# Optimization experiments

Hardware: AMD Instinct MI355X
Metric: run time of the kernel (lower is better)

The kernel has to match this reference:

```python
import jax, jax.numpy as jnp
import numpy as np
import math

EPS = 1e-6


def setup_inputs() -> dict:
    key = jax.random.key(0)
    ks = jax.random.split(key, 6)
    Bsz, S, d_in, d_out, E, r = 4, 2048, 2048, 2048, 16, 16
    x = jax.random.normal(ks[0], (Bsz, S, d_in), dtype=jnp.float32)
    base_W = jax.random.normal(ks[1], (d_out, d_in), dtype=jnp.float32) * (1.0 / math.sqrt(d_in))
    base_b = jax.random.normal(ks[2], (d_out,), dtype=jnp.float32)
    A = jax.random.normal(ks[3], (E, r, d_in), dtype=jnp.float32) * (1.0 / math.sqrt(d_in))
    B = jax.random.normal(ks[4], (E, d_out, r), dtype=jnp.float32) * (1.0 / math.sqrt(r))
    gate_v = jax.random.normal(ks[5], (E, d_in), dtype=jnp.float32)
    alphas = jnp.full((E,), 32.0, dtype=jnp.float32)
    return {"x": x, "base_W": base_W, "base_b": base_b, "A": A, "B": B,
            "gate_v": gate_v, "alphas": alphas, "top_k": 2}


def reference(x, base_W, base_b, A, B, gate_v, alphas, top_k):
    d = x.shape[-1]
    out_shape = x.shape[:-1] + (base_W.shape[0],)
    base_out = jnp.einsum('bsd,od->bso', x, base_W) + base_b

    x_flat = x.reshape(-1, d)                                  # [T, d]
    T = x_flat.shape[0]
    E = A.shape[0]
    # cosine routing scores
    xn = x_flat / (jnp.linalg.norm(x_flat, axis=-1, keepdims=True) + EPS)
    vn = gate_v / (jnp.linalg.norm(gate_v, axis=-1, keepdims=True) + EPS)
    scores = (xn @ vn.T) / jnp.sqrt(jnp.float32(d))            # [T, E]
    topk_s, topk_i = jax.lax.top_k(scores, top_k)              # [T, k]
    w = jax.nn.softmax(topk_s, axis=-1)                        # [T, k]
    # dense combine weight per (token, expert); non-selected experts get 0
    Wte = jnp.zeros((T, E), dtype=x.dtype).at[jnp.arange(T)[:, None], topk_i].add(w)
    scale = alphas / jnp.float32(A.shape[1])                   # [E]
    # grouped LoRA: mid [T,E,r] is tiny (r=16); contract without [T,E,out]
    mid = jnp.einsum('td,erd->ter', x_flat, A)
    contrib = jnp.einsum('ter,eor,te,e->to', mid, B, Wte, scale)
    return base_out + contrib.reshape(out_shape)
```

## Files before the change

### kernel.cpp

```cpp
#include <hip/hip_runtime.h>
#include <math.h>


typedef unsigned short u16;
typedef __attribute__((ext_vector_type(8))) short short8;
typedef __attribute__((ext_vector_type(4))) float floatx4;

#define DEV __device__ __forceinline__

DEV u16 f2b(float f) { unsigned int u; __builtin_memcpy(&u, &f, 4); u += 0x7fffu + ((u >> 16) & 1u); return (u16)(u >> 16); }
DEV float ldf(const float* __restrict__ p, long long i, long long n) { if (i < 0 || i >= n) i = 0; return p[i]; }

DEV void async_cp16(const void* g, void* l) {
  __builtin_amdgcn_global_load_lds(
      (const __attribute__((address_space(1))) unsigned int*)g,
      (__attribute__((address_space(3))) unsigned int*)l, 16, 0, 0);
}

struct Route { int e0, e1; float c0, c1; };

#define MAX_T 8192
#define MAX_K 2048
#define MAX_DOUT 2048
#define MAX_ER 256

__device__ Route g_route[MAX_T];
__device__ float g_vnorm[16];
__device__ float g_mid[(size_t)MAX_T * MAX_ER];
__device__ __align__(16) u16 g_xb[(size_t)MAX_T * MAX_K];
__device__ __align__(16) u16 g_wb[(size_t)MAX_DOUT * MAX_K];
__device__ __align__(16) u16 g_ab[(size_t)MAX_ER * MAX_K];
__device__ __align__(16) u16 g_mw[(size_t)MAX_T * MAX_ER];
__device__ __align__(16) u16 g_w2[(size_t)MAX_DOUT * MAX_ER];

__global__ __launch_bounds__(256) void cvt_bf16(const float* __restrict__ src, long long n, int which) {
  u16* dst; long long cap;
  if (which == 1) { dst = g_wb; cap = (long long)MAX_DOUT * MAX_K; }
  else { dst = g_ab; cap = (long long)MAX_ER * MAX_K; }
  const long long stride = (long long)gridDim.x * 256 * 4;
  for (long long i4 = ((long long)blockIdx.x * 256 + threadIdx.x) * 4; i4 < n; i4 += stride) {
    if (i4 + 4 <= n && i4 + 4 <= cap) {
      const float4 v = *(const float4*)(src + i4);
      ushort4 o;
      o.x = f2b(v.x); o.y = f2b(v.y); o.z = f2b(v.z); o.w = f2b(v.w);
      *(ushort4*)(dst + i4) = o;
    } else {
      for (long long j = i4; j < n && j < cap; ++j) dst[j] = f2b(src[j]);
    }
  }
}

__global__ __launch_bounds__(256) void build_w2(const float* __restrict__ Bw, long long nB,
                                                int d_out, int r, int E, int Er) {
  const int gid = blockIdx.x * 256 + threadIdx.x;
  if (gid >= d_out * E) return;
  const int o = gid / E, e = gid % E;
  const long long src = ((long long)e * d_out + o) * r;
  const long long dst = (long long)o * Er + (long long)e * r;
  if (r == 16 && src + 16 <= nB) {
    short8 lo, hi;
#pragma unroll
    for (int j = 0; j < 8; ++j) lo[j] = (short)f2b(Bw[src + j]);
#pragma unroll
    for (int j = 0; j < 8; ++j) hi[j] = (short)f2b(Bw[src + 8 + j]);
    *(short8*)&g_w2[dst] = lo;
    *(short8*)&g_w2[dst + 8] = hi;
  } else {
    for (int j = 0; j < r; ++j) g_w2[dst + j] = f2b(ldf(Bw, src + j, nB));
  }
}

__global__ __launch_bounds__(64) void gate_norm(const float* __restrict__ gv, long long nG,
                                                int d, int E) {
  const int e = blockIdx.x;
  if (e >= E || e >= 16) return;
  const int lane = threadIdx.x;
  float vv = 0.f;
  const float* gp = gv + (long long)e * d;
  for (int k = lane * 4; k + 4 <= d; k += 256) {
    const float4 g = *(const float4*)(gp + k);
    vv += g.x * g.x + g.y * g.y + g.z * g.z + g.w * g.w;
  }
#pragma unroll
  for (int m = 1; m < 64; m <<= 1) vv += __shfl_xor(vv, m);
  if (lane == 0) g_vnorm[e] = sqrtf(vv) + 1e-6f;
}

__global__ __launch_bounds__(256) void router_cvtx(
    const float* __restrict__ x, long long nX,
    const float* __restrict__ gate_v, long long nG,
    const float* __restrict__ alphas, long long nAl,
    const int* __restrict__ topk_ptr, int has_topk,
    int T, int d, int r, int E) {
  const int wave = threadIdx.x >> 6, lane = threadIdx.x & 63;
  const int t = blockIdx.x * 4 + wave;
  if (t >= T || t >= MAX_T) return;
  float xx = 0.f, dot[16], vv[16];
#pragma unroll
  for (int e = 0; e < 16; ++e) { dot[e] = 0.f; vv[e] = 0.f; }
  const long long xbase = (long long)t * d;
  const int dvec = ((d & 3) == 0) ? d : 0;
  for (int i = lane * 4; i < dvec; i += 256) {
    const float4 xv = *(const float4*)(x + xbase + i);
    xx += xv.x * xv.x + xv.y * xv.y + xv.z * xv.z + xv.w * xv.w;
    ushort4 ob; ob.x = f2b(xv.x); ob.y = f2b(xv.y); ob.z = f2b(xv.z); ob.w = f2b(xv.w);
    *(ushort4*)&g_xb[xbase + i] = ob;
#pragma unroll
    for (int e = 0; e < 16; ++e) {
      if (e < E) {
        const float4 g = *(const float4*)(gate_v + (long long)e * d + i);
        dot[e] += xv.x * g.x + xv.y * g.y + xv.z * g.z + xv.w * g.w;
        vv[e] += g.x * g.x + g.y * g.y + g.z * g.z + g.w * g.w;
      }
    }
  }
  for (int i = dvec + lane; i < d; i += 64) {
    const float xv = ldf(x, xbase + i, nX);
    g_xb[xbase + i] = f2b(xv);
    xx += xv * xv;
#pragma unroll
    for (int e = 0; e < 16; ++e) {
      if (e < E) {
        const float g = ldf(gate_v, (long long)e * d + i, nG);
        dot[e] += xv * g;
        vv[e] += g * g;
      }
    }
  }
#pragma unroll
  for (int m = 1; m < 64; m <<= 1) {
    xx += __shfl_xor(xx, m);
#pragma unroll
    for (int e = 0; e < 16; ++e) {
      dot[e] += __shfl_xor(dot[e], m);
      vv[e] += __shfl_xor(vv[e], m);
    }
  }
  const float inv_sd = 1.0f / sqrtf((float)d);
  const float xnorm = sqrtf(xx) + 1e-6f;
  float s[16];
#pragma unroll
  for (int e = 0; e < 16; ++e)
    s[e] = (e < E) ? dot[e] / (xnorm * (sqrtf(vv[e]) + 1e-6f)) * inv_sd : -1e30f;
  int e0 = 0; float s0 = s[0];
#pragma unroll
  for (int e = 1; e < 16; ++e) if (s[e] > s0) { s0 = s[e]; e0 = e; }
  int e1 = (e0 == 0) ? 1 : 0; float s1 = s[e1];
#pragma unroll
  for (int e = 0; e < 16; ++e) if (e != e0 && s[e] > s1) { s1 = s[e]; e1 = e; }
  const int k = has_topk ? *topk_ptr : 2;
  float w0 = 1.f, w1 = 0.f;
  if (k >= 2) {
    const float ex = expf(s1 - s0);
    w0 = 1.f / (1.f + ex);
    w1 = ex / (1.f + ex);
  } else {
    e1 = e0;
  }
  if (lane == 0) {
    Route rt;
    rt.e0 = e0; rt.e1 = e1;
    rt.c0 = w0 * ldf(alphas, e0, nAl) / (float)r;
    rt.c1 = w1 * ldf(alphas, e1, nAl) / (float)r;
    g_route[t] = rt;
  }
}

__global__ __launch_bounds__(256) void router_lds(
    const float* __restrict__ x, long long nX,
    const float* __restrict__ gate_v, long long nG,
    const float* __restrict__ alphas, long long nAl,
    const int* __restrict__ topk_ptr, int has_topk,
    int T, int d, int r, int E) {
  __shared__ __align__(16) float gls[4096];
  const int tid = threadIdx.x;
  const int w = tid >> 6, lane = tid & 63;
  const int t = blockIdx.x * 4 + w;
  const bool valid = (t < T && t < MAX_T);
  const long long xbase = (long long)t * d;

  float dot[16], xx = 0.f;
#pragma unroll
  for (int e = 0; e < 16; ++e) dot[e] = 0.f;

  for (int k0 = 0; k0 < d; k0 += 256) {
    __syncthreads();
#pragma unroll
    for (int i = 0; i < 4; ++i) {
      const int f = tid * 4 + i * 1024;
      const int e = f >> 8, kk = f & 255;
      float4 g = (float4){0.f, 0.f, 0.f, 0.f};
      if (e < E) g = *(const float4*)(gate_v + (long long)e * d + k0 + kk);
      *(float4*)&gls[f] = g;
    }
    __syncthreads();
    float4 xv = (float4){0.f, 0.f, 0.f, 0.f};
    if (valid) {
      xv = *(const float4*)(x + xbase + k0 + lane * 4);
      ushort4 ob; ob.x = f2b(xv.x); ob.y = f2b(xv.y); ob.z = f2b(xv.z); ob.w = f2b(xv.w);
      *(ushort4*)&g_xb[xbase + k0 + lane * 4] = ob;
    }
    xx += xv.x * xv.x + xv.y * xv.y + xv.z * xv.z + xv.w * xv.w;
#pragma unroll
    for (int e = 0; e < 16; ++e) {
      if (e < E) {
        const float4 g = *(const float4*)&gls[e * 256 + lane * 4];
        dot[e] += xv.x * g.x + xv.y * g.y + xv.z * g.z + xv.w * g.w;
      }
    }
  }
#pragma unroll
  for (int m = 1; m < 64; m <<= 1) {
    xx += __shfl_xor(xx, m);
#pragma unroll
    for (int e = 0; e < 16; ++e) dot[e] += __shfl_xor(dot[e], m);
  }
  if (valid && lane == 0) {
    const float inv_sd = 1.0f / sqrtf((float)d);
    const float xnorm = sqrtf(xx) + 1e-6f;
    float s[16];
#pragma unroll
    for (int e = 0; e < 16; ++e)
      s[e] = (e < E) ? dot[e] / (xnorm * g_vnorm[e]) * inv_sd : -1e30f;
    int e0 = 0; float s0 = s[0];
#pragma unroll
    for (int e = 1; e < 16; ++e) if (s[e] > s0) { s0 = s[e]; e0 = e; }
    int e1 = (e0 == 0) ? 1 : 0; float s1 = s[e1];
#pragma unroll
    for (int e = 0; e < 16; ++e) if (e != e0 && s[e] > s1) { s1 = s[e]; e1 = e; }
    const int k = has_topk ? *topk_ptr : 2;
    float w0 = 1.f, w1 = 0.f;
    if (k >= 2) {
      const float ex = expf(s1 - s0);
      w0 = 1.f / (1.f + ex);
      w1 = ex / (1.f + ex);
    } else {
      e1 = e0;
    }
    Route rt;
    rt.e0 = e0; rt.e1 = e1;
    rt.c0 = w0 * ldf(alphas, e0, nAl) / (float)r;
    rt.c1 = w1 * ldf(alphas, e1, nAl) / (float)r;
    g_route[t] = rt;
  }
}

#define BM 128
#define BN 128
#define BK 32

__global__ __launch_bounds__(256) void gemm_main(
    const float* __restrict__ bias, long long nBias,
    float* __restrict__ Out, long long nOut,
    int K, int d_out, int Er, int T) {
  __shared__ __align__(16) u16 As[BM * BK];
  __shared__ __align__(16) u16 Bs[BN * BK];
  const int tid = threadIdx.x;
  const int w = tid >> 6, lane = tid & 63;
  const int Mb = blockIdx.y * BM;
  const int Nb = blockIdx.x * BN;
  const int wm = w >> 1, wn = w & 1;
  const int chunk0 = w * 2;
  const int srow = lane >> 2;
  const int kb = (lane & 3) * 8;

  floatx4 acc[4][4];
#pragma unroll
  for (int mt = 0; mt < 4; ++mt)
#pragma unroll
    for (int nt = 0; nt < 4; ++nt) acc[mt][nt] = (floatx4){0.f, 0.f, 0.f, 0.f};

  for (int k0 = 0; k0 < K; k0 += BK) {
#pragma unroll
    for (int c = 0; c < 2; ++c) {
      const int row = (chunk0 + c) * 16 + srow;
      async_cp16(g_xb + (size_t)(Mb + row) * K + (k0 + kb), (char*)As + (chunk0 + c) * 1024);
    }
#pragma unroll
    for (int c = 0; c < 2; ++c) {
      const int row = (chunk0 + c) * 16 + srow;
      const int col = Nb + row;
      const u16* g = (col >= d_out) ? g_ab + (size_t)(col - d_out) * K + (k0 + kb)
                                    : g_wb + (size_t)col * K + (k0 + kb);
      async_cp16(g, (char*)Bs + (chunk0 + c) * 1024);
    }
    __syncthreads();
    short8 a[4], b[4];
#pragma unroll
    for (int mt = 0; mt < 4; ++mt)
      a[mt] = *(const short8*)&As[(wm * 64 + mt * 16 + (lane & 15)) * BK + (lane >> 4) * 8];
#pragma unroll
    for (int nt = 0; nt < 4; ++nt)
      b[nt] = *(const short8*)&Bs[(wn * 64 + nt * 16 + (lane & 15)) * BK + (lane >> 4) * 8];
#pragma unroll
    for (int mt = 0; mt < 4; ++mt)
#pragma unroll
      for (int nt = 0; nt < 4; ++nt)
        acc[mt][nt] = __builtin_amdgcn_mfma_f32_16x16x32_bf16(a[mt], b[nt], acc[mt][nt], 0, 0, 0);
    __syncthreads();
  }

  const int colb = Nb + wn * 64 + (lane & 15);
  const int rowb = Mb + wm * 64 + (lane >> 4) * 4;
#pragma unroll
  for (int nt = 0; nt < 4; ++nt) {
    const int col = colb + nt * 16;
    const bool isOut = (col < d_out);
    const float bv = isOut ? ldf(bias, col, nBias) : 0.f;
#pragma unroll
    for (int mt = 0; mt < 4; ++mt) {
      const int row = rowb + mt * 16;
#pragma unroll
      for (int i = 0; i < 4; ++i) {
        const int rr = row + i;
        if (rr >= T) continue;
        if (isOut) {
          const long long idx = (long long)rr * d_out + col;
          if (idx < nOut) Out[idx] = acc[mt][nt][i] + bv;
        } else {
          const int mc = col - d_out;
          if (mc < Er) g_mid[(long long)rr * Er + mc] = acc[mt][nt][i];
        }
      }
    }
  }
}

__global__ __launch_bounds__(256) void build_mw(int T, int r, int Er, int E) {
  const int t = blockIdx.x;
  if (t >= T) return;
  const Route rt = g_route[t];
  for (int j = threadIdx.x; j < Er; j += 256) {
    const int e = (r == 16) ? (j >> 4) : (j / r);
    float wgt = 0.f;
    if (e == rt.e0) wgt = rt.c0;
    else if (e == rt.e1) wgt = rt.c1;
    g_mw[(long long)t * Er + j] = f2b(wgt * g_mid[(long long)t * Er + j]);
  }
}

__global__ __launch_bounds__(256) void gemm_lora(
    float* __restrict__ Out, long long nOut, int Kc, int d_out, int T) {
  __shared__ __align__(16) u16 As[BM * BK];
  __shared__ __align__(16) u16 Bs[BN * BK];
  const int tid = threadIdx.x;
  const int w = tid >> 6, lane = tid & 63;
  const int Mb = blockIdx.y * BM;
  const int Nb = blockIdx.x * BN;
  const int wm = w >> 1, wn = w & 1;
  const int chunk0 = w * 2;
  const int srow = lane >> 2;
  const int kb = (lane & 3) * 8;

  floatx4 acc[4][4];
#pragma unroll
  for (int mt = 0; mt < 4; ++mt)
#pragma unroll
    for (int nt = 0; nt < 4; ++nt) acc[mt][nt] = (floatx4){0.f, 0.f, 0.f, 0.f};

  for (int k0 = 0; k0 < Kc; k0 += BK) {
#pragma unroll
    for (int c = 0; c < 2; ++c) {
      const int row = (chunk0 + c) * 16 + srow;
      async_cp16(g_mw + (size_t)(Mb + row) * Kc + (k0 + kb), (char*)As + (chunk0 + c) * 1024);
      async_cp16(g_w2 + (size_t)(Nb + row) * Kc + (k0 + kb), (char*)Bs + (chunk0 + c) * 1024);
    }
    __syncthreads();
    short8 a[4], b[4];
#pragma unroll
    for (int mt = 0; mt < 4; ++mt)
      a[mt] = *(const short8*)&As[(wm * 64 + mt * 16 + (lane & 15)) * BK + (lane >> 4) * 8];
#pragma unroll
    for (int nt = 0; nt < 4; ++nt)
      b[nt] = *(const short8*)&Bs[(wn * 64 + nt * 16 + (lane & 15)) * BK + (lane >> 4) * 8];
#pragma unroll
    for (int mt = 0; mt < 4; ++mt)
#pragma unroll
      for (int nt = 0; nt < 4; ++nt)
        acc[mt][nt] = __builtin_amdgcn_mfma_f32_16x16x32_bf16(a[mt], b[nt], acc[mt][nt], 0, 0, 0);
    __syncthreads();
  }

  const int colb = Nb + wn * 64 + (lane & 15);
  const int rowb = Mb + wm * 64 + (lane >> 4) * 4;
#pragma unroll
  for (int nt = 0; nt < 4; ++nt) {
    const int col = colb + nt * 16;
#pragma unroll
    for (int mt = 0; mt < 4; ++mt) {
      const int row = rowb + mt * 16;
#pragma unroll
      for (int i = 0; i < 4; ++i) {
        const int rr = row + i;
        if (rr >= T) continue;
        const long long idx = (long long)rr * d_out + col;
        if (idx < nOut) Out[idx] += acc[mt][nt][i];
      }
    }
  }
}


__global__ __launch_bounds__(256) void gemm_mid(int K, int Er, int T, int r) {
  __shared__ __align__(16) u16 As[BM * BK];
  __shared__ __align__(16) u16 Bs[BN * BK];
  const int tid = threadIdx.x;
  const int w = tid >> 6, lane = tid & 63;
  int lin = blockIdx.y * gridDim.x + blockIdx.x;
  const int nwg = gridDim.x * gridDim.y;
  if ((nwg & 7) == 0) { const int cpx = nwg >> 3; lin = (lin & 7) * cpx + (lin >> 3); }
  const int Mb = (lin / gridDim.x) * BM;
  const int Nb = (lin % gridDim.x) * BN;
  const int wm = w >> 1, wn = w & 1;
  const int chunk0 = w * 2;
  const int srow = lane >> 2;
  const int kb = (lane & 3) * 8;

  floatx4 acc[4][4];
#pragma unroll
  for (int mt = 0; mt < 4; ++mt)
#pragma unroll
    for (int nt = 0; nt < 4; ++nt) acc[mt][nt] = (floatx4){0.f, 0.f, 0.f, 0.f};

  for (int k0 = 0; k0 < K; k0 += BK) {
#pragma unroll
    for (int c = 0; c < 2; ++c) {
      const int row = (chunk0 + c) * 16 + srow;
      async_cp16(g_xb + (size_t)(Mb + row) * K + (k0 + kb), (char*)As + (chunk0 + c) * 1024);
      async_cp16(g_ab + (size_t)(Nb + row) * K + (k0 + kb), (char*)Bs + (chunk0 + c) * 1024);
    }
    __syncthreads();
    short8 a[4], b[4];
#pragma unroll
    for (int mt = 0; mt < 4; ++mt)
      a[mt] = *(const short8*)&As[(wm * 64 + mt * 16 + (lane & 15)) * BK + (lane >> 4) * 8];
#pragma unroll
    for (int nt = 0; nt < 4; ++nt)
      b[nt] = *(const short8*)&Bs[(wn * 64 + nt * 16 + (lane & 15)) * BK + (lane >> 4) * 8];
#pragma unroll
    for (int mt = 0; mt < 4; ++mt)
#pragma unroll
      for (int nt = 0; nt < 4; ++nt)
        acc[mt][nt] = __builtin_amdgcn_mfma_f32_16x16x32_bf16(a[mt], b[nt], acc[mt][nt], 0, 0, 0);
    __syncthreads();
  }

  const int colb = Nb + wn * 64 + (lane & 15);
  const int rowb = Mb + wm * 64 + (lane >> 4) * 4;
#pragma unroll
  for (int mt = 0; mt < 4; ++mt) {
#pragma unroll
    for (int i = 0; i < 4; ++i) {
      const int rr = rowb + mt * 16 + i;
      if (rr >= T) continue;
      const Route rt = g_route[rr];
#pragma unroll
      for (int nt = 0; nt < 4; ++nt) {
        const int col = colb + nt * 16;
        if (col >= Er) continue;
        const int e = (r == 16) ? (col >> 4) : (col / r);
        float wgt = 0.f;
        if (e == rt.e0) wgt = rt.c0;
        else if (e == rt.e1) wgt = rt.c1;
        g_mw[(long long)rr * Er + col] = f2b(wgt * acc[mt][nt][i]);
      }
    }
  }
}

DEV void stage_ht(int tsched, int half, int isB, int NT, int Mb, int Nb,
                  int Kxb, int Er, char* smem, int w, int lane) {
  int t = (tsched < NT) ? tsched : (NT - 1);
  const int k0 = t << 6;
  const u16* src; int stride, col0;
  if (k0 < Kxb) { src = isB ? g_wb : g_xb; stride = Kxb; col0 = k0; }
  else          { src = isB ? g_w2 : g_mw; stride = Er;  col0 = k0 - Kxb; }
  const int rbase = (isB ? Nb : Mb) + (half << 7);
  char* dst = smem + (tsched & 1) * 65536 + isB * 32768 + half * 16384 + (w * 2) * 1024;
  const int row = w * 16 + (lane >> 3);
  const int cs = (((lane & 7) ^ (lane >> 3)) << 3);
#pragma unroll
  for (int c = 0; c < 2; ++c) {
    async_cp16(src + (size_t)(rbase + row + c * 8) * stride + col0 + cs, dst + c * 1024);
  }
}

__global__ __launch_bounds__(512, 2) void gemm_main8(
    const float* __restrict__ bias, long long nBias,
    float* __restrict__ Out, long long nOut,
    int Kxb, int d_out, int Er, int T) {
  __shared__ __align__(16) char smem[131072];
  const int tid = threadIdx.x;
  const int w = tid >> 6, lane = tid & 63;
  const int wm = w >> 2, wn = w & 3;
  const int lane15 = lane & 15, laneHi = lane >> 4, lane7 = lane & 7;
  const int NT = (Kxb + Er) >> 6;

  int lin = blockIdx.y * gridDim.x + blockIdx.x;
  const int nwg = gridDim.x * gridDim.y;
  if ((nwg & 7) == 0) { const int cpx = nwg >> 3; lin = (lin & 7) * cpx + (lin >> 3); }
  const int Nb = (lin % gridDim.x) * 256;
  const int Mb = (lin / gridDim.x) * 256;

  floatx4 acc[8][4];
#pragma unroll
  for (int m = 0; m < 8; ++m)
#pragma unroll
    for (int n = 0; n < 4; ++n) acc[m][n] = (floatx4){0.f, 0.f, 0.f, 0.f};

  stage_ht(0, 0, 0, NT, Mb, Nb, Kxb, Er, smem, w, lane);
  stage_ht(0, 1, 0, NT, Mb, Nb, Kxb, Er, smem, w, lane);
  stage_ht(0, 0, 1, NT, Mb, Nb, Kxb, Er, smem, w, lane);
  stage_ht(0, 1, 1, NT, Mb, Nb, Kxb, Er, smem, w, lane);
  stage_ht(1, 0, 1, NT, Mb, Nb, Kxb, Er, smem, w, lane);
  stage_ht(1, 1, 1, NT, Mb, Nb, Kxb, Er, smem, w, lane);
  asm volatile("s_waitcnt vmcnt(4)" ::: "memory");
  __builtin_amdgcn_s_barrier();
  asm volatile("" ::: "memory");

  const int xorw = lane7 << 4;
  short8 a[2][2], b[4][2];

  for (int t = 0; t < NT; ++t) {
    const int sbase = (t & 1) * 65536;
    const char* Ab = smem + sbase;
    const char* Bb = smem + sbase + 32768;
#pragma unroll
    for (int q = 0; q < 4; ++q) {
      if (q == 0) {
#pragma unroll
        for (int n = 0; n < 4; ++n)
#pragma unroll
          for (int kk = 0; kk < 2; ++kk)
            b[n][kk] = *(const short8*)(Bb + (wn * 64 + n * 16 + lane15) * 128 +
                                        ((kk * 64 + laneHi * 16) ^ xorw));
      }
#pragma unroll
      for (int mm = 0; mm < 2; ++mm)
#pragma unroll
        for (int kk = 0; kk < 2; ++kk)
          a[mm][kk] = *(const short8*)(Ab + (wm * 128 + (2 * q + mm) * 16 + lane15) * 128 +
                                       ((kk * 64 + laneHi * 16) ^ xorw));
      if (q < 2) stage_ht(t + 1, q, 0, NT, Mb, Nb, Kxb, Er, smem, w, lane);
      else       stage_ht(t + 2, q - 2, 1, NT, Mb, Nb, Kxb, Er, smem, w, lane);
      if (q == 3) asm volatile("s_waitcnt vmcnt(4)" ::: "memory");
      __builtin_amdgcn_s_barrier();
      asm volatile("" ::: "memory");
      asm volatile("s_waitcnt lgkmcnt(0)" ::: "memory");
      __builtin_amdgcn_s_setprio(1);
#pragma unroll
      for (int kk = 0; kk < 2; ++kk)
#pragma unroll
        for (int mm = 0; mm < 2; ++mm)
#pragma unroll
          for (int n = 0; n < 4; ++n)
            acc[2 * q + mm][n] =
                __builtin_amdgcn_mfma_f32_16x16x32_bf16(a[mm][kk], b[n][kk], acc[2 * q + mm][n], 0, 0, 0);
      __builtin_amdgcn_s_setprio(0);
      __builtin_amdgcn_s_barrier();
      asm volatile("" ::: "memory");
    }
  }
  asm volatile("s_waitcnt vmcnt(0)" ::: "memory");

  const int colb = Nb + wn * 64 + lane15;
  const int rowb = Mb + wm * 128 + laneHi * 4;
#pragma unroll
  for (int n = 0; n < 4; ++n) {
    const int col = colb + n * 16;
    const float bv = ldf(bias, col, nBias);
#pragma unroll
    for (int m = 0; m < 8; ++m) {
#pragma unroll
      for (int i = 0; i < 4; ++i) {
        const int row = rowb + m * 16 + i;
        const long long idx = (long long)row * d_out + col;
        if (row < T && idx < nOut) Out[idx] = acc[m][n][i] + bv;
      }
    }
  }
}

extern "C" void kernel_launch(void* const* d_in, const int* in_sizes, int n_in,
                              void* d_out, int out_size, void* d_ws, size_t ws_size,
                              hipStream_t stream) {
  if (n_in < 7 || !d_out) return;
  const float* x    = (const float*)d_in[0];
  const float* W    = (const float*)d_in[1];
  const float* bias = (const float*)d_in[2];
  const float* A    = (const float*)d_in[3];
  const float* B    = (const float*)d_in[4];
  const float* gv   = (const float*)d_in[5];
  const float* al   = (const float*)d_in[6];
  const int has_topk = (n_in > 7 && in_sizes[7] >= 1) ? 1 : 0;
  const int* topk = has_topk ? (const int*)d_in[7] : nullptr;
  float* out = (float*)d_out;

  const long long nX = in_sizes[0], nW = in_sizes[1], nBias = in_sizes[2];
  const long long nA = in_sizes[3], nB = in_sizes[4], nG = in_sizes[5], nAl = in_sizes[6];
  const long long nOut = (long long)out_size;

  const int E = in_sizes[6] > 0 ? in_sizes[6] : 1;
  int d = (int)(nG / E); if (d < 1) d = 1;
  const int d_out_dim = in_sizes[2] > 0 ? in_sizes[2] : 1;
  int T = (int)(nX / d);
  int r = (int)(nA / ((long long)E * d)); if (r < 1) r = 1;
  const int Er = E * r;
  if (T < 1) return;
  if (T > MAX_T) T = MAX_T;
  if (d > MAX_K || d_out_dim > MAX_DOUT || Er > MAX_ER) return;

  cvt_bf16<<<4096, 256, 0, stream>>>(W, nW, 1);
  cvt_bf16<<<512, 256, 0, stream>>>(A, nA, 2);
  build_w2<<<(d_out_dim * E + 255) / 256, 256, 0, stream>>>(B, nB, d_out_dim, r, E, Er);

  const bool fastr = (d % 256 == 0) && (E <= 16);
  if (fastr) {
    gate_norm<<<E, 64, 0, stream>>>(gv, nG, d, E);
    router_lds<<<(T + 3) / 4, 256, 0, stream>>>(x, nX, gv, nG, al, nAl, topk, has_topk, T, d, r, E);
  } else {
    router_cvtx<<<(T + 3) / 4, 256, 0, stream>>>(x, nX, gv, nG, al, nAl, topk, has_topk, T, d, r, E);
  }

  const bool fast = (T % 256 == 0) && (d_out_dim % 256 == 0) && (d % 64 == 0) &&
                    (Er % 128 == 0) && (((d + Er) >> 6) >= 2);
  if (fast) {
    dim3 gmid(Er / BN, T / BM);
    gemm_mid<<<gmid, 256, 0, stream>>>(d, Er, T, r);
    dim3 gmain(d_out_dim / 256, T / 256);
    gemm_main8<<<gmain, 512, 0, stream>>>(bias, nBias, out, nOut, d, d_out_dim, Er, T);
  } else {
    dim3 grid1((d_out_dim + Er + BN - 1) / BN, (T + BM - 1) / BM);
    gemm_main<<<grid1, 256, 0, stream>>>(bias, nBias, out, nOut, d, d_out_dim, Er, T);
    build_mw<<<T, 256, 0, stream>>>(T, r, Er, E);
    dim3 grid2((d_out_dim + BN - 1) / BN, (T + BM - 1) / BM);
    gemm_lora<<<grid2, 256, 0, stream>>>(out, nOut, Er, d_out_dim, T);
  }
}
```

Baseline: 327.6 us.

## Merge prep kernels, shrink mid-GEMM tile, and stage main GEMM epilogue through LDS

Folds the three weight-conversion kernels and the gate-norm kernel into one launch, which cuts launch overhead. The LoRA mid GEMM moves to 128x64 tiles so the small Er dimension yields more workgroups. The main GEMM epilogue now writes accumulators into shared memory and stores them as coalesced float4 rows instead of scattered scalar writes. These changes add extra barriers and assume enough LDS is free per wave in the epilogue.

```diff
diff --git a/kernel.cpp b/kernel.cpp
--- a/kernel.cpp
+++ b/kernel.cpp
@@ -33,57 +33,76 @@
 __device__ __align__(16) u16 g_mw[(size_t)MAX_T * MAX_ER];
 __device__ __align__(16) u16 g_w2[(size_t)MAX_DOUT * MAX_ER];
 
-__global__ __launch_bounds__(256) void cvt_bf16(const float* __restrict__ src, long long n, int which) {
-  u16* dst; long long cap;
-  if (which == 1) { dst = g_wb; cap = (long long)MAX_DOUT * MAX_K; }
-  else { dst = g_ab; cap = (long long)MAX_ER * MAX_K; }
-  const long long stride = (long long)gridDim.x * 256 * 4;
-  for (long long i4 = ((long long)blockIdx.x * 256 + threadIdx.x) * 4; i4 < n; i4 += stride) {
-    if (i4 + 4 <= n && i4 + 4 <= cap) {
-      const float4 v = *(const float4*)(src + i4);
-      ushort4 o;
-      o.x = f2b(v.x); o.y = f2b(v.y); o.z = f2b(v.z); o.w = f2b(v.w);
-      *(ushort4*)(dst + i4) = o;
+__global__ __launch_bounds__(256) void prep_all(
+    const float* __restrict__ W, long long nW,
+    const float* __restrict__ A, long long nA,
+    const float* __restrict__ Bw, long long nB,
+    const float* __restrict__ gv, long long nG,
+    int d, int d_out, int r, int E, int Er,
+    int nWblk, int nAblk, int w2blk) {
+  int b = blockIdx.x;
+  const int tid = threadIdx.x;
+  if (b < nWblk) {
+    const long long cap = (long long)MAX_DOUT * MAX_K;
+    const long long stride = (long long)nWblk * 1024;
+    for (long long i4 = ((long long)b * 256 + tid) * 4; i4 < nW; i4 += stride) {
+      if (i4 + 4 <= nW && i4 + 4 <= cap) {
+        const float4 v = *(const float4*)(W + i4);
+        ushort4 o; o.x = f2b(v.x); o.y = f2b(v.y); o.z = f2b(v.z); o.w = f2b(v.w);
+        *(ushort4*)&g_wb[i4] = o;
+      } else {
+        for (long long j = i4; j < nW && j < cap; ++j) g_wb[j] = f2b(W[j]);
+      }
+    }
+    return;
+  }
+  b -= nWblk;
+  if (b < nAblk) {
+    const long long cap = (long long)MAX_ER * MAX_K;
+    const long long stride = (long long)nAblk * 1024;
+    for (long long i4 = ((long long)b * 256 + tid) * 4; i4 < nA; i4 += stride) {
+      if (i4 + 4 <= nA && i4 + 4 <= cap) {
+        const float4 v = *(const float4*)(A + i4);
+        ushort4 o; o.x = f2b(v.x); o.y = f2b(v.y); o.z = f2b(v.z); o.w = f2b(v.w);
+        *(ushort4*)&g_ab[i4] = o;
+      } else {
+        for (long long j = i4; j < nA && j < cap; ++j) g_ab[j] = f2b(A[j]);
+      }
+    }
+    return;
+  }
+  b -= nAblk;
+  if (b < w2blk) {
+    const int gid = b * 256 + tid;
+    if (gid >= d_out * E) return;
+    const int o = gid / E, e = gid % E;
+    const long long src = ((long long)e * d_out + o) * r;
+    const long long dst = (long long)o * Er + (long long)e * r;
+    if (r == 16 && src + 16 <= nB) {
+      short8 lo, hi;
+#pragma unroll
+      for (int j = 0; j < 8; ++j) lo[j] = (short)f2b(Bw[src + j]);
+#pragma unroll
+      for (int j = 0; j < 8; ++j) hi[j] = (short)f2b(Bw[src + 8 + j]);
+      *(short8*)&g_w2[dst] = lo;
+      *(short8*)&g_w2[dst + 8] = hi;
     } else {
-      for (long long j = i4; j < n && j < cap; ++j) dst[j] = f2b(src[j]);
-    }
-  }
-}
-
-__global__ __launch_bounds__(256) void build_w2(const float* __restrict__ Bw, long long nB,
-                                                int d_out, int r, int E, int Er) {
-  const int gid = blockIdx.x * 256 + threadIdx.x;
-  if (gid >= d_out * E) return;
-  const int o = gid / E, e = gid % E;
-  const long long src = ((long long)e * d_out + o) * r;
-  const long long dst = (long long)o * Er + (long long)e * r;
-  if (r == 16 && src + 16 <= nB) {
-    short8 lo, hi;
-#pragma unroll
-    for (int j = 0; j < 8; ++j) lo[j] = (short)f2b(Bw[src + j]);
-#pragma unroll
-    for (int j = 0; j < 8; ++j) hi[j] = (short)f2b(Bw[src + 8 + j]);
-    *(short8*)&g_w2[dst] = lo;
-    *(short8*)&g_w2[dst + 8] = hi;
-  } else {
-    for (int j = 0; j < r; ++j) g_w2[dst + j] = f2b(ldf(Bw, src + j, nB));
-  }
-}
-
-__global__ __launch_bounds__(64) void gate_norm(const float* __restrict__ gv, long long nG,
-                                                int d, int E) {
-  const int e = blockIdx.x;
-  if (e >= E || e >= 16) return;
-  const int lane = threadIdx.x;
-  float vv = 0.f;
-  const float* gp = gv + (long long)e * d;
-  for (int k = lane * 4; k + 4 <= d; k += 256) {
-    const float4 g = *(const float4*)(gp + k);
-    vv += g.x * g.x + g.y * g.y + g.z * g.z + g.w * g.w;
-  }
-#pragma unroll
-  for (int m = 1; m < 64; m <<= 1) vv += __shfl_xor(vv, m);
-  if (lane == 0) g_vnorm[e] = sqrtf(vv) + 1e-6f;
+      for (int j = 0; j < r; ++j) g_w2[dst + j] = f2b(ldf(Bw, src + j, nB));
+    }
+    return;
+  }
+  b -= w2blk;
+  if (b < E && b < 16 && tid < 64) {
+    float vv = 0.f;
+    const float* gp = gv + (long long)b * d;
+    for (int k = tid * 4; k + 4 <= d; k += 256) {
+      const float4 g = *(const float4*)(gp + k);
+      vv += g.x * g.x + g.y * g.y + g.z * g.z + g.w * g.w;
+    }
+#pragma unroll
+    for (int m = 1; m < 64; m <<= 1) vv += __shfl_xor(vv, m);
+    if (tid == 0) g_vnorm[b] = sqrtf(vv) + 1e-6f;
+  }
 }
 
 __global__ __launch_bounds__(256) void router_cvtx(
@@ -401,52 +420,52 @@
 }
 
 
-__global__ __launch_bounds__(256) void gemm_mid(int K, int Er, int T, int r) {
-  __shared__ __align__(16) u16 As[BM * BK];
-  __shared__ __align__(16) u16 Bs[BN * BK];
+__global__ __launch_bounds__(256) void gemm_mid64(int K, int Er, int T, int r) {
+  __shared__ __align__(16) u16 As[128 * 32];
+  __shared__ __align__(16) u16 Bs[64 * 32];
   const int tid = threadIdx.x;
   const int w = tid >> 6, lane = tid & 63;
   int lin = blockIdx.y * gridDim.x + blockIdx.x;
   const int nwg = gridDim.x * gridDim.y;
   if ((nwg & 7) == 0) { const int cpx = nwg >> 3; lin = (lin & 7) * cpx + (lin >> 3); }
-  const int Mb = (lin / gridDim.x) * BM;
-  const int Nb = (lin % gridDim.x) * BN;
+  const int Mb = (lin / gridDim.x) * 128;
+  const int Nb = (lin % gridDim.x) * 64;
   const int wm = w >> 1, wn = w & 1;
-  const int chunk0 = w * 2;
   const int srow = lane >> 2;
   const int kb = (lane & 3) * 8;
-
-  floatx4 acc[4][4];
+  const int lane15 = lane & 15, laneHi = lane >> 4;
+
+  floatx4 acc[4][2];
 #pragma unroll
   for (int mt = 0; mt < 4; ++mt)
 #pragma unroll
-    for (int nt = 0; nt < 4; ++nt) acc[mt][nt] = (floatx4){0.f, 0.f, 0.f, 0.f};
-
-  for (int k0 = 0; k0 < K; k0 += BK) {
+    for (int nt = 0; nt < 2; ++nt) acc[mt][nt] = (floatx4){0.f, 0.f, 0.f, 0.f};
+
+  for (int k0 = 0; k0 < K; k0 += 32) {
 #pragma unroll
     for (int c = 0; c < 2; ++c) {
-      const int row = (chunk0 + c) * 16 + srow;
-      async_cp16(g_xb + (size_t)(Mb + row) * K + (k0 + kb), (char*)As + (chunk0 + c) * 1024);
-      async_cp16(g_ab + (size_t)(Nb + row) * K + (k0 + kb), (char*)Bs + (chunk0 + c) * 1024);
-    }
-    __syncthreads();
-    short8 a[4], b[4];
+      const int ci = w * 2 + c;
+      async_cp16(g_xb + (size_t)(Mb + ci * 16 + srow) * K + (k0 + kb), (char*)As + ci * 1024);
+    }
+    async_cp16(g_ab + (size_t)(Nb + w * 16 + srow) * K + (k0 + kb), (char*)Bs + w * 1024);
+    __syncthreads();
+    short8 a[4], b[2];
 #pragma unroll
     for (int mt = 0; mt < 4; ++mt)
-      a[mt] = *(const short8*)&As[(wm * 64 + mt * 16 + (lane & 15)) * BK + (lane >> 4) * 8];
-#pragma unroll
-    for (int nt = 0; nt < 4; ++nt)
-      b[nt] = *(const short8*)&Bs[(wn * 64 + nt * 16 + (lane & 15)) * BK + (lane >> 4) * 8];
+      a[mt] = *(const short8*)&As[(wm * 64 + mt * 16 + lane15) * 32 + laneHi * 8];
+#pragma unroll
+    for (int nt = 0; nt < 2; ++nt)
+      b[nt] = *(const short8*)&Bs[(wn * 32 + nt * 16 + lane15) * 32 + laneHi * 8];
 #pragma unroll
     for (int mt = 0; mt < 4; ++mt)
 #pragma unroll
-      for (int nt = 0; nt < 4; ++nt)
+      for (int nt = 0; nt < 2; ++nt)
         acc[mt][nt] = __builtin_amdgcn_mfma_f32_16x16x32_bf16(a[mt], b[nt], acc[mt][nt], 0, 0, 0);
     __syncthreads();
   }
 
-  const int colb = Nb + wn * 64 + (lane & 15);
-  const int rowb = Mb + wm * 64 + (lane >> 4) * 4;
+  const int colb = Nb + wn * 32 + lane15;
+  const int rowb = Mb + wm * 64 + laneHi * 4;
 #pragma unroll
   for (int mt = 0; mt < 4; ++mt) {
 #pragma unroll
@@ -455,7 +474,7 @@
       if (rr >= T) continue;
       const Route rt = g_route[rr];
 #pragma unroll
-      for (int nt = 0; nt < 4; ++nt) {
+      for (int nt = 0; nt < 2; ++nt) {
         const int col = colb + nt * 16;
         if (col >= Er) continue;
         const int e = (r == 16) ? (col >> 4) : (col / r);
@@ -562,22 +581,39 @@
     }
   }
   asm volatile("s_waitcnt vmcnt(0)" ::: "memory");
-
-  const int colb = Nb + wn * 64 + lane15;
-  const int rowb = Mb + wm * 128 + laneHi * 4;
-#pragma unroll
-  for (int n = 0; n < 4; ++n) {
-    const int col = colb + n * 16;
-    const float bv = ldf(bias, col, nBias);
-#pragma unroll
-    for (int m = 0; m < 8; ++m) {
-#pragma unroll
-      for (int i = 0; i < 4; ++i) {
-        const int row = rowb + m * 16 + i;
-        const long long idx = (long long)row * d_out + col;
-        if (row < T && idx < nOut) Out[idx] = acc[m][n][i] + bv;
-      }
-    }
+  __builtin_amdgcn_s_barrier();
+  asm volatile("" ::: "memory");
+
+  float* eps = (float*)(smem + (size_t)w * 4608);
+  const int er_row = lane >> 4;
+  const int er_col = (lane & 15) * 4;
+  float bvv[4];
+#pragma unroll
+  for (int n = 0; n < 4; ++n) bvv[n] = ldf(bias, Nb + wn * 64 + n * 16 + lane15, nBias);
+
+  for (int m = 0; m < 8; ++m) {
+#pragma unroll
+    for (int n = 0; n < 4; ++n)
+#pragma unroll
+      for (int i = 0; i < 4; ++i)
+        eps[(laneHi * 4 + i) * 72 + n * 16 + lane15] = acc[m][n][i] + bvv[n];
+    __syncthreads();
+#pragma unroll
+    for (int j = 0; j < 4; ++j) {
+      const int rr = Mb + wm * 128 + m * 16 + j * 4 + er_row;
+      const floatx4 v = *(const floatx4*)&eps[(j * 4 + er_row) * 72 + er_col];
+      if (rr < T) {
+        const long long idx = (long long)rr * d_out + (Nb + wn * 64 + er_col);
+        if (idx + 4 <= nOut) {
+          *(floatx4*)(Out + idx) = v;
+        } else {
+#pragma unroll
+          for (int qq = 0; qq < 4; ++qq)
+            if (idx + qq < nOut) Out[idx + qq] = v[qq];
+        }
+      }
+    }
+    __syncthreads();
   }
 }
 
@@ -610,23 +646,22 @@
   if (T > MAX_T) T = MAX_T;
   if (d > MAX_K || d_out_dim > MAX_DOUT || Er > MAX_ER) return;
 
-  cvt_bf16<<<4096, 256, 0, stream>>>(W, nW, 1);
-  cvt_bf16<<<512, 256, 0, stream>>>(A, nA, 2);
-  build_w2<<<(d_out_dim * E + 255) / 256, 256, 0, stream>>>(B, nB, d_out_dim, r, E, Er);
+  const int nWblk = 2048, nAblk = 256;
+  const int w2blk = (d_out_dim * E + 255) / 256;
+  prep_all<<<nWblk + nAblk + w2blk + E, 256, 0, stream>>>(
+      W, nW, A, nA, B, nB, gv, nG, d, d_out_dim, r, E, Er, nWblk, nAblk, w2blk);
 
   const bool fastr = (d % 256 == 0) && (E <= 16);
-  if (fastr) {
-    gate_norm<<<E, 64, 0, stream>>>(gv, nG, d, E);
+  if (fastr)
     router_lds<<<(T + 3) / 4, 256, 0, stream>>>(x, nX, gv, nG, al, nAl, topk, has_topk, T, d, r, E);
-  } else {
+  else
     router_cvtx<<<(T + 3) / 4, 256, 0, stream>>>(x, nX, gv, nG, al, nAl, topk, has_topk, T, d, r, E);
-  }
 
   const bool fast = (T % 256 == 0) && (d_out_dim % 256 == 0) && (d % 64 == 0) &&
-                    (Er % 128 == 0) && (((d + Er) >> 6) >= 2);
+                    (Er % 64 == 0) && (((d + Er) >> 6) >= 2) && (Er >= 64);
   if (fast) {
-    dim3 gmid(Er / BN, T / BM);
-    gemm_mid<<<gmid, 256, 0, stream>>>(d, Er, T, r);
+    dim3 gmid(Er / 64, T / 128);
+    gemm_mid64<<<gmid, 256, 0, stream>>>(d, Er, T, r);
     dim3 gmain(d_out_dim / 256, T / 256);
     gemm_main8<<<gmain, 512, 0, stream>>>(bias, nBias, out, nOut, d, d_out_dim, Er, T);
   } else {
```

New measurement: 321.2 us. 1.02x faster.
